# Performance work log

Hardware: AMD Instinct MI355X
Metric: run time of the kernel (lower is better)

## Reference

```python
import jax, jax.numpy as jnp
import numpy as np

B, S, HID = 1, 2048, 3584
NH, NKV, HD = 16, 8, 256
WIN = 1024                      # sliding_window_size
SOFTCAP = 50.0                  # attn_logit_softcapping
SCALING = 256 ** -0.5           # query_pre_attn_scalar ** -0.5
NEG = -2.3819763e38


def setup_inputs() -> dict:
    key = jax.random.key(0)
    k1, k2, k3 = jax.random.split(key, 3)
    hidden_states = jax.random.normal(k1, (B, S, HID), dtype=jnp.float32)
    Wqkv = jax.random.normal(k2, (HID, (NH + 2 * NKV) * HD), dtype=jnp.float32) * 0.02
    Wo = jax.random.normal(k3, (NH * HD, HID), dtype=jnp.float32) * 0.02
    # RoPE angles: freqs_cis = exp(i * pos * inv_freq), passed as cos/sin [S, HD/2]
    inv_freq = 1.0 / (10000.0 ** (jnp.arange(0, HD, 2, dtype=jnp.float32) / HD))
    ang = jnp.arange(S, dtype=jnp.float32)[:, None] * inv_freq[None, :]
    freqs_cos, freqs_sin = jnp.cos(ang), jnp.sin(ang)
    # causal additive mask [1,1,S,S]
    i = jnp.arange(S)
    mask = jnp.where(i[None, :] <= i[:, None], 0.0, NEG)[None, None, :, :].astype(jnp.float32)
    return {"hidden_states": hidden_states, "Wqkv": Wqkv, "Wo": Wo,
            "freqs_cos": freqs_cos, "freqs_sin": freqs_sin, "mask": mask}


def _rope(x, cos, sin):
    # x: [B,S,H,D]; complex mult on (first_half + i*second_half), real->first half, imag->second
    x1, x2 = jnp.split(x, 2, axis=-1)
    c = cos[None, :, None, :]
    s = sin[None, :, None, :]
    return jnp.concatenate([x1 * c - x2 * s, x1 * s + x2 * c], axis=-1)


def reference(hidden_states, Wqkv, Wo, freqs_cos, freqs_sin, mask):
    qkv = hidden_states @ Wqkv                                   # [B,S,(NH+2*NKV)*HD]
    xq, xk, xv = jnp.split(qkv, [NH * HD, (NH + NKV) * HD], axis=-1)
    xq = xq.reshape(B, S, NH, HD)
    xk = xk.reshape(B, S, NKV, HD)
    xv = xv.reshape(B, S, NKV, HD)
    xq = _rope(xq, freqs_cos, freqs_sin)
    xk = _rope(xk, freqs_cos, freqs_sin)
    g = NH // NKV                                                # GQA repeat_interleave
    k = jnp.repeat(xk, g, axis=2)                                # [B,S,NH,HD]
    v = jnp.repeat(xv, g, axis=2)
    scores = jnp.einsum('bqhd,bkhd->bhqk', xq * SCALING, k)      # [B,NH,S,S]
    # sliding-window band: triu(-W+1) * tril(W-1)  <=>  |i-j| < W
    i = jnp.arange(S)
    band = jnp.abs(i[:, None] - i[None, :]) < WIN
    m = jnp.where(band[None, None, :, :], mask, NEG)
    scores = jnp.tanh(scores / SOFTCAP) * SOFTCAP + m            # logit softcapping
    probs = jax.nn.softmax(scores.astype(jnp.float32), axis=-1).astype(xq.dtype)
    out = jnp.einsum('bhqk,bkhd->bqhd', probs, v).reshape(B, S, NH * HD)
    return out @ Wo
```

## Files before the change

kernel.cpp:

```cpp
#include <hip/hip_runtime.h>
#include <hip/hip_bf16.h>
#include <stdint.h>

#define S_LEN 2048
#define HIDDEN 3584
#define NHEAD 16
#define NKVH 8
#define HDIM 256
#define QKV_N 8192
#define AO_N 4096
#define WINLEN 1024

typedef __attribute__((ext_vector_type(8))) short bf16x8;
typedef __attribute__((ext_vector_type(4))) float f32x4;

__device__ __forceinline__ void async_cp16(const void* g, void* l) {
  __builtin_amdgcn_global_load_lds(
      (const __attribute__((address_space(1))) void*)g,
      (__attribute__((address_space(3))) void*)l, 16, 0, 0);
}

__device__ __forceinline__ float fast_exp2(float x) {
#if __has_builtin(__builtin_amdgcn_exp2f)
  return __builtin_amdgcn_exp2f(x);
#else
  return __exp2f(x);
#endif
}
__device__ __forceinline__ float fast_rcp(float x) {
#if __has_builtin(__builtin_amdgcn_rcpf)
  return __builtin_amdgcn_rcpf(x);
#else
  return 1.0f / x;
#endif
}

__device__ __forceinline__ unsigned short f2bf(float f) {
  unsigned u = __float_as_uint(f);
  u += 0x7FFF + ((u >> 16) & 1);
  return (unsigned short)(u >> 16);
}
__device__ __forceinline__ float bf2f(unsigned short h) {
  return __uint_as_float(((unsigned)h) << 16);
}

__global__ void k_cast_bf16(const float* __restrict__ in,
                            unsigned short* __restrict__ out, int n4) {
  int i = blockIdx.x * blockDim.x + threadIdx.x;
  int stride = gridDim.x * blockDim.x;
  for (; i < n4; i += stride) {
    float4 v = ((const float4*)in)[i];
    uint2 o;
    o.x = (unsigned)f2bf(v.x) | ((unsigned)f2bf(v.y) << 16);
    o.y = (unsigned)f2bf(v.z) | ((unsigned)f2bf(v.w) << 16);
    ((uint2*)out)[i] = o;
  }
}

__global__ void k_transpose_bf16(const float* __restrict__ in,
                                 unsigned short* __restrict__ out,
                                 int R, int C) {
  __shared__ float tile[64][65];
  int c0 = blockIdx.x * 64, r0 = blockIdx.y * 64;
  int t = threadIdx.x;
#pragma unroll
  for (int j = 0; j < 16; ++j) {
    int idx = t + j * 256;
    int rl = idx >> 6, cl = idx & 63;
    tile[rl][cl] = in[(size_t)(r0 + rl) * C + c0 + cl];
  }
  __syncthreads();
#pragma unroll
  for (int j = 0; j < 16; ++j) {
    int idx = t + j * 256;
    int cl = idx >> 6, rl = idx & 63;
    out[(size_t)(c0 + cl) * R + r0 + rl] = f2bf(tile[rl][cl]);
  }
}

template <bool OUT_BF16>
__global__ __launch_bounds__(256, 2) void k_gemm(
    const unsigned short* __restrict__ A, const unsigned short* __restrict__ B,
    void* __restrict__ Cout, int M, int N, int K) {
  __shared__ unsigned short sA[2][128 * 64];
  __shared__ unsigned short sB[2][128 * 64];
  const int t = threadIdx.x;
  const int lane = t & 63;
  const int wid = t >> 6;
  const int m0 = blockIdx.y * 128;
  const int n0 = blockIdx.x * 128;
  const int wr = wid >> 1, wc = wid & 1;
  const int lrow = lane & 15, lgrp = lane >> 4;

  f32x4 acc[4][4] = {};

  const int lr = lane >> 3;
  const int sw = (lane & 7) ^ (lr & 7);

  const int NT = K >> 6;

  auto stage = [&](int buf, int kt) {
    const int klo = kt * 64;
#pragma unroll
    for (int i = 0; i < 4; ++i) {
      int r = wid * 32 + i * 8 + lr;
      async_cp16(A + (size_t)(m0 + r) * K + klo + sw * 8,
                 &sA[buf][(wid * 32 + i * 8) * 64]);
    }
#pragma unroll
    for (int i = 0; i < 4; ++i) {
      int r = wid * 32 + i * 8 + lr;
      async_cp16(B + (size_t)(n0 + r) * K + klo + sw * 8,
                 &sB[buf][(wid * 32 + i * 8) * 64]);
    }
  };

  stage(0, 0);
  for (int kt = 0; kt < NT; ++kt) {
    int cur = kt & 1;
    __syncthreads();
    if (kt + 1 < NT) stage(cur ^ 1, kt + 1);
#pragma unroll
    for (int kk = 0; kk < 2; ++kk) {
      bf16x8 af[4], bfr[4];
#pragma unroll
      for (int m = 0; m < 4; ++m) {
        int r = wr * 64 + m * 16 + lrow;
        int c = (kk * 4 + lgrp) ^ (r & 7);
        af[m] = *(const bf16x8*)&sA[cur][r * 64 + c * 8];
      }
#pragma unroll
      for (int n = 0; n < 4; ++n) {
        int r = wc * 64 + n * 16 + lrow;
        int c = (kk * 4 + lgrp) ^ (r & 7);
        bfr[n] = *(const bf16x8*)&sB[cur][r * 64 + c * 8];
      }
#pragma unroll
      for (int m = 0; m < 4; ++m)
#pragma unroll
        for (int n = 0; n < 4; ++n)
          acc[m][n] = __builtin_amdgcn_mfma_f32_16x16x32_bf16(
              af[m], bfr[n], acc[m][n], 0, 0, 0);
    }
  }
#pragma unroll
  for (int m = 0; m < 4; ++m) {
    int row_b = m0 + wr * 64 + m * 16 + lgrp * 4;
#pragma unroll
    for (int n = 0; n < 4; ++n) {
      int col = n0 + wc * 64 + n * 16 + lrow;
#pragma unroll
      for (int r = 0; r < 4; ++r) {
        int row = row_b + r;
        if constexpr (OUT_BF16)
          ((unsigned short*)Cout)[(size_t)row * N + col] = f2bf(acc[m][n][r]);
        else
          ((float*)Cout)[(size_t)row * N + col] = acc[m][n][r];
      }
    }
  }
}

__global__ void k_rope_layout(const unsigned short* __restrict__ qkv,
                              const float* __restrict__ fcos,
                              const float* __restrict__ fsin,
                              unsigned short* __restrict__ Q,
                              unsigned short* __restrict__ K,
                              unsigned short* __restrict__ VT) {
  int s0 = blockIdx.x * 64;
  int y = blockIdx.y;
  int t = threadIdx.x;
  if (y < 24) {
    int colb = (y < 16) ? y * 256 : 4096 + (y - 16) * 256;
    unsigned short* out =
        (y < 16) ? (Q + (size_t)y * S_LEN * HDIM)
                 : (K + (size_t)(y - 16) * S_LEN * HDIM);
#pragma unroll 4
    for (int j = 0; j < 32; ++j) {
      int idx = t + j * 256;
      int sl = idx >> 7;
      int d = idx & 127;
      int s = s0 + sl;
      float x1 = bf2f(qkv[(size_t)s * QKV_N + colb + d]);
      float x2 = bf2f(qkv[(size_t)s * QKV_N + colb + d + 128]);
      float c = fcos[s * 128 + d], sn = fsin[s * 128 + d];
      out[(size_t)s * HDIM + d] = f2bf(x1 * c - x2 * sn);
      out[(size_t)s * HDIM + d + 128] = f2bf(x1 * sn + x2 * c);
    }
  } else {
    int kh = y - 24;
    __shared__ unsigned short tile[64][258];
#pragma unroll 4
    for (int j = 0; j < 64; ++j) {
      int idx = t + j * 256;
      int sl = idx >> 8;
      int d = idx & 255;
      tile[sl][d] = qkv[(size_t)(s0 + sl) * QKV_N + 6144 + kh * 256 + d];
    }
    __syncthreads();
    size_t base = (size_t)kh * HDIM * S_LEN + (size_t)(s0 >> 6) * (HDIM * 64);
#pragma unroll 4
    for (int j = 0; j < 64; ++j) {
      int idx = t + j * 256;
      int d = idx >> 6;
      int sl = idx & 63;
      VT[base + idx] = tile[sl][d];
    }
  }
}

__global__ __launch_bounds__(256, 2) void k_attn(
    const unsigned short* __restrict__ Q,
    const unsigned short* __restrict__ K,
    const unsigned short* __restrict__ VTB,
    unsigned short* __restrict__ O) {
  __shared__ unsigned short sK[64 * 256];
  __shared__ unsigned short sV[256 * 64];
  __shared__ unsigned short sP[4][16 * 64];
  const int t = threadIdx.x, lane = t & 63, w = t >> 6;
  const int h = blockIdx.y;
  const int r0b = blockIdx.x * 64;
  const int r0w = r0b + w * 16;
  const int lrow = lane & 15, lgrp = lane >> 4;
  const unsigned short* Qh = Q + (size_t)h * S_LEN * HDIM;
  const char* KhB = (const char*)(K + (size_t)(h >> 1) * S_LEN * HDIM);
  const char* VbB = (const char*)(VTB + (size_t)(h >> 1) * S_LEN * HDIM);

  const int cK = t & 31;
  const int rK = t >> 5;
  const int csK = (cK & 24) | ((cK ^ rK) & 7);
  const int ksrcoff = rK * 512 + csK * 16;
  const int csV = (t & 7) ^ ((t >> 3) & 7);
  const int vsrcoff = (t >> 3) * 128 + csV * 16;

  bf16x8 qf[8];
#pragma unroll
  for (int dc = 0; dc < 8; ++dc)
    qf[dc] =
        *(const bf16x8*)&Qh[(size_t)(r0w + lrow) * HDIM + dc * 32 + lgrp * 8];

  f32x4 zero4 = {0.f, 0.f, 0.f, 0.f};
  f32x4 o[16];
#pragma unroll
  for (int i = 0; i < 16; ++i) o[i] = zero4;
  float psum[4] = {0.f, 0.f, 0.f, 0.f};

  const int klo = (r0b >= 1024) ? (r0b - 1024) : 0;
  const int nsteps = ((r0b - klo) >> 6) + 1;

  const float c_pre = 0.0625f / 50.0f;
  const float c_2l2e = 2.8853900817779268f;
  const float c_l2e = 1.4426950408889634f;
  unsigned short* myP = sP[w];

  for (int step = 0; step < nsteps; ++step) {
    const int k0 = klo + step * 64;
    __syncthreads();
    {
      const char* ks = KhB + (size_t)k0 * 512;
      const char* vs = VbB + (size_t)(k0 >> 6) * 32768;
      char* dK = (char*)sK + t * 16;
      char* dV = (char*)sV + t * 16;
#pragma unroll
      for (int rr = 0; rr < 8; ++rr)
        async_cp16(ks + ksrcoff + rr * 4096, dK + rr * 4096);
#pragma unroll
      for (int rr = 0; rr < 8; ++rr)
        async_cp16(vs + vsrcoff + rr * 4096, dV + rr * 4096);
    }
    __syncthreads();

#pragma unroll
    for (int st = 0; st < 4; ++st) {
      const int row = st * 16 + lrow;
      const int rs7 = lrow & 7;
      f32x4 sa = zero4, sb = zero4;
#pragma unroll
      for (int dc = 0; dc < 4; ++dc) {
        const int La = dc * 4 + lgrp;
        const int Lb = (dc + 4) * 4 + lgrp;
        bf16x8 kfa = *(const bf16x8*)&sK[row * 256 +
                                         ((La & 24) | ((La ^ rs7) & 7)) * 8];
        bf16x8 kfb = *(const bf16x8*)&sK[row * 256 +
                                         ((Lb & 24) | ((Lb ^ rs7) & 7)) * 8];
        sa = __builtin_amdgcn_mfma_f32_16x16x32_bf16(qf[dc], kfa, sa, 0, 0, 0);
        sb = __builtin_amdgcn_mfma_f32_16x16x32_bf16(qf[dc + 4], kfb, sb, 0, 0,
                                                     0);
      }
      f32x4 s = sa + sb;
#pragma unroll
      for (int r = 0; r < 4; ++r) {
        const int q = r0w + lgrp * 4 + r;
        const int k = k0 + st * 16 + lrow;
        float tt = s[r] * c_pre;
        tt = fminf(fmaxf(tt, -10.f), 10.f);
        float z = fast_exp2(tt * c_2l2e);
        float sc = (z - 1.f) * fast_rcp(z + 1.f) * 50.f;
        float p = 0.f;
        if (k <= q && (q - k) < WINLEN)
          p = fast_exp2((sc - 50.f) * c_l2e);
        unsigned short pb = f2bf(p);
        psum[r] += bf2f(pb);
        const int qrow = lgrp * 4 + r;
        const int cc = st * 2 + (lrow >> 3);
        myP[qrow * 64 + (cc ^ (qrow & 7)) * 8 + (lrow & 7)] = pb;
      }
    }

#pragma unroll
    for (int ks2 = 0; ks2 < 2; ++ks2) {
      const int cc = ks2 * 4 + lgrp;
      bf16x8 pf = *(const bf16x8*)&myP[lrow * 64 + (cc ^ (lrow & 7)) * 8];
#pragma unroll
      for (int dt = 0; dt < 16; ++dt) {
        const int d = dt * 16 + lrow;
        bf16x8 vf = *(const bf16x8*)&sV[d * 64 + (cc ^ (lrow & 7)) * 8];
        o[dt] = __builtin_amdgcn_mfma_f32_16x16x32_bf16(pf, vf, o[dt], 0, 0, 0);
      }
    }
  }

#pragma unroll
  for (int r = 0; r < 4; ++r) {
    float v = psum[r];
    v += __shfl_xor(v, 1);
    v += __shfl_xor(v, 2);
    v += __shfl_xor(v, 4);
    v += __shfl_xor(v, 8);
    psum[r] = 1.0f / v;
  }
#pragma unroll
  for (int dt = 0; dt < 16; ++dt)
#pragma unroll
    for (int r = 0; r < 4; ++r) {
      int row = r0w + lgrp * 4 + r;
      O[(size_t)row * AO_N + h * HDIM + dt * 16 + lrow] =
          f2bf(o[dt][r] * psum[r]);
    }
}

extern "C" void kernel_launch(void* const* d_in, const int* in_sizes, int n_in,
                              void* d_out, int out_size, void* d_ws,
                              size_t ws_size, hipStream_t stream) {
  const float* hidden = (const float*)d_in[0];
  const float* Wqkv = (const float*)d_in[1];
  const float* Wo = (const float*)d_in[2];
  const float* fcos = (const float*)d_in[3];
  const float* fsin = (const float*)d_in[4];
  float* out = (float*)d_out;
  char* ws = (char*)d_ws;

  unsigned short* WqkvT = (unsigned short*)(ws + 0);
  unsigned short* hb = (unsigned short*)(ws + 58720256);
  unsigned short* qkv = (unsigned short*)(ws + 73400320);
  unsigned short* WoT = (unsigned short*)(ws + 106954752);
  unsigned short* Qb = WqkvT;
  unsigned short* Kb = WqkvT + (size_t)16 * 2048 * 256;
  unsigned short* VTb = WqkvT + (size_t)24 * 2048 * 256;
  unsigned short* AO = qkv;

  k_cast_bf16<<<1024, 256, 0, stream>>>(hidden, hb, (2048 * 3584) / 4);
  k_transpose_bf16<<<dim3(8192 / 64, 3584 / 64), 256, 0, stream>>>(
      Wqkv, WqkvT, 3584, 8192);
  k_transpose_bf16<<<dim3(3584 / 64, 4096 / 64), 256, 0, stream>>>(
      Wo, WoT, 4096, 3584);
  k_gemm<true><<<dim3(64, 16), 256, 0, stream>>>(hb, WqkvT, qkv, 2048, 8192,
                                                 3584);
  k_rope_layout<<<dim3(32, 32), 256, 0, stream>>>(qkv, fcos, fsin, Qb, Kb, VTb);
  k_attn<<<dim3(32, 16), 256, 0, stream>>>(Qb, Kb, VTb, AO);
  k_gemm<false><<<dim3(28, 16), 256, 0, stream>>>(AO, WoT, out, 2048, 3584,
                                                  4096);
}
```

Before: 564.6 us.

## Replace GEMM with larger-tile 512-thread kernel with grid swizzle and MFMA priority

Both projection GEMMs move to a new kernel with 256-wide N tiles (BM 256 for QKV, 128 for output), 8 waves per block, and a swizzled block ordering meant to improve L2 reuse. The inner loop splits fragment loads into quadrants with explicit vmcnt waits, raw barriers, and s_setprio around MFMA bursts to overlap LDS reads with matrix math. Occupancy drops to one 512-thread block per CU, and the hand-written waitcnt and barrier sequence is fragile.

```diff
diff --git a/kernel.cpp b/kernel.cpp
--- a/kernel.cpp
+++ b/kernel.cpp
@@ -42,6 +42,12 @@
 }
 __device__ __forceinline__ float bf2f(unsigned short h) {
   return __uint_as_float(((unsigned)h) << 16);
+}
+
+__device__ __forceinline__ void bar() {
+  asm volatile("" ::: "memory");
+  __builtin_amdgcn_s_barrier();
+  asm volatile("" ::: "memory");
 }
 
 __global__ void k_cast_bf16(const float* __restrict__ in,
@@ -78,84 +84,153 @@
   }
 }
 
-template <bool OUT_BF16>
-__global__ __launch_bounds__(256, 2) void k_gemm(
+template <int BM, bool OUT_BF16>
+__global__ __launch_bounds__(512, 1) void k_gemm2(
     const unsigned short* __restrict__ A, const unsigned short* __restrict__ B,
     void* __restrict__ Cout, int M, int N, int K) {
-  __shared__ unsigned short sA[2][128 * 64];
-  __shared__ unsigned short sB[2][128 * 64];
+  constexpr int M_REP = BM / 32;
+  constexpr int HM = M_REP / 2;
+  constexpr int LPK = BM / 64 + 4;
+  __shared__ unsigned short sA[2][BM * 64];
+  __shared__ unsigned short sB[2][256 * 64];
   const int t = threadIdx.x;
   const int lane = t & 63;
   const int wid = t >> 6;
-  const int m0 = blockIdx.y * 128;
-  const int n0 = blockIdx.x * 128;
-  const int wr = wid >> 1, wc = wid & 1;
+  const int wr = wid >> 2, wc = wid & 3;
   const int lrow = lane & 15, lgrp = lane >> 4;
 
-  f32x4 acc[4][4] = {};
-
-  const int lr = lane >> 3;
-  const int sw = (lane & 7) ^ (lr & 7);
+  const int gx = gridDim.x;
+  const int nwg = gx * gridDim.y;
+  const int bid = blockIdx.y * gx + blockIdx.x;
+  const int swz = (bid & 7) * (nwg >> 3) + (bid >> 3);
+  const int m0 = (swz / gx) * BM;
+  const int n0 = (swz % gx) * 256;
 
   const int NT = K >> 6;
 
-  auto stage = [&](int buf, int kt) {
-    const int klo = kt * 64;
-#pragma unroll
-    for (int i = 0; i < 4; ++i) {
-      int r = wid * 32 + i * 8 + lr;
-      async_cp16(A + (size_t)(m0 + r) * K + klo + sw * 8,
-                 &sA[buf][(wid * 32 + i * 8) * 64]);
-    }
-#pragma unroll
-    for (int i = 0; i < 4; ++i) {
-      int r = wid * 32 + i * 8 + lr;
-      async_cp16(B + (size_t)(n0 + r) * K + klo + sw * 8,
-                 &sB[buf][(wid * 32 + i * 8) * 64]);
-    }
+  const int sr = t >> 3;
+  const int scs = ((t & 7) ^ (sr & 7)) * 8;
+  auto stage = [&](int kt, int buf) {
+    const size_t kb = (size_t)kt * 64;
+    unsigned short* dA = &sA[buf][sr * 64 + (t & 7) * 8];
+    unsigned short* dB = &sB[buf][sr * 64 + (t & 7) * 8];
+#pragma unroll
+    for (int l = 0; l < BM / 64; ++l)
+      async_cp16(A + (size_t)(m0 + l * 64 + sr) * K + kb + scs,
+                 dA + l * 64 * 64);
+#pragma unroll
+    for (int l = 0; l < 4; ++l)
+      async_cp16(B + (size_t)(n0 + l * 64 + sr) * K + kb + scs,
+                 dB + l * 64 * 64);
   };
+
+  f32x4 acc[M_REP][4] = {};
 
   stage(0, 0);
   for (int kt = 0; kt < NT; ++kt) {
-    int cur = kt & 1;
-    __syncthreads();
-    if (kt + 1 < NT) stage(cur ^ 1, kt + 1);
-#pragma unroll
-    for (int kk = 0; kk < 2; ++kk) {
-      bf16x8 af[4], bfr[4];
-#pragma unroll
-      for (int m = 0; m < 4; ++m) {
-        int r = wr * 64 + m * 16 + lrow;
-        int c = (kk * 4 + lgrp) ^ (r & 7);
-        af[m] = *(const bf16x8*)&sA[cur][r * 64 + c * 8];
-      }
-#pragma unroll
-      for (int n = 0; n < 4; ++n) {
-        int r = wc * 64 + n * 16 + lrow;
-        int c = (kk * 4 + lgrp) ^ (r & 7);
-        bfr[n] = *(const bf16x8*)&sB[cur][r * 64 + c * 8];
-      }
-#pragma unroll
-      for (int m = 0; m < 4; ++m)
-#pragma unroll
-        for (int n = 0; n < 4; ++n)
-          acc[m][n] = __builtin_amdgcn_mfma_f32_16x16x32_bf16(
-              af[m], bfr[n], acc[m][n], 0, 0, 0);
-    }
-  }
-#pragma unroll
-  for (int m = 0; m < 4; ++m) {
-    int row_b = m0 + wr * 64 + m * 16 + lgrp * 4;
-#pragma unroll
-    for (int n = 0; n < 4; ++n) {
-      int col = n0 + wc * 64 + n * 16 + lrow;
+    const int buf = kt & 1;
+    if (kt + 1 < NT) {
+      stage(kt + 1, buf ^ 1);
+      if constexpr (LPK == 8)
+        asm volatile("s_waitcnt vmcnt(8)" ::: "memory");
+      else
+        asm volatile("s_waitcnt vmcnt(6)" ::: "memory");
+    } else {
+      asm volatile("s_waitcnt vmcnt(0)" ::: "memory");
+    }
+    bar();
+
+    const unsigned short* a = sA[buf];
+    const unsigned short* b = sB[buf];
+    auto ldA = [&](int mf, int kk) {
+      return *(const bf16x8*)&a[(wr * (BM / 2) + mf * 16 + lrow) * 64 +
+                                (((kk * 4 + lgrp)) ^ (lrow & 7)) * 8];
+    };
+    auto ldB = [&](int nf, int kk) {
+      return *(const bf16x8*)&b[(wc * 64 + nf * 16 + lrow) * 64 +
+                                (((kk * 4 + lgrp)) ^ (lrow & 7)) * 8];
+    };
+
+    bf16x8 aA[HM][2], bB0[2][2], bB1[2][2];
+#pragma unroll
+    for (int i = 0; i < HM; ++i) {
+      aA[i][0] = ldA(i, 0);
+      aA[i][1] = ldA(i, 1);
+    }
+#pragma unroll
+    for (int j = 0; j < 2; ++j) {
+      bB0[j][0] = ldB(j, 0);
+      bB0[j][1] = ldB(j, 1);
+    }
+    __builtin_amdgcn_s_setprio(1);
+#pragma unroll
+    for (int i = 0; i < HM; ++i)
+#pragma unroll
+      for (int j = 0; j < 2; ++j)
+#pragma unroll
+        for (int kk = 0; kk < 2; ++kk)
+          acc[i][j] = __builtin_amdgcn_mfma_f32_16x16x32_bf16(
+              aA[i][kk], bB0[j][kk], acc[i][j], 0, 0, 0);
+    __builtin_amdgcn_s_setprio(0);
+    bar();
+#pragma unroll
+    for (int j = 0; j < 2; ++j) {
+      bB1[j][0] = ldB(2 + j, 0);
+      bB1[j][1] = ldB(2 + j, 1);
+    }
+    __builtin_amdgcn_s_setprio(1);
+#pragma unroll
+    for (int i = 0; i < HM; ++i)
+#pragma unroll
+      for (int j = 0; j < 2; ++j)
+#pragma unroll
+        for (int kk = 0; kk < 2; ++kk)
+          acc[i][2 + j] = __builtin_amdgcn_mfma_f32_16x16x32_bf16(
+              aA[i][kk], bB1[j][kk], acc[i][2 + j], 0, 0, 0);
+    __builtin_amdgcn_s_setprio(0);
+    bar();
+#pragma unroll
+    for (int i = 0; i < HM; ++i) {
+      aA[i][0] = ldA(HM + i, 0);
+      aA[i][1] = ldA(HM + i, 1);
+    }
+    __builtin_amdgcn_s_setprio(1);
+#pragma unroll
+    for (int i = 0; i < HM; ++i)
+#pragma unroll
+      for (int j = 0; j < 2; ++j)
+#pragma unroll
+        for (int kk = 0; kk < 2; ++kk)
+          acc[HM + i][2 + j] = __builtin_amdgcn_mfma_f32_16x16x32_bf16(
+              aA[i][kk], bB1[j][kk], acc[HM + i][2 + j], 0, 0, 0);
+    __builtin_amdgcn_s_setprio(0);
+    bar();
+    __builtin_amdgcn_s_setprio(1);
+#pragma unroll
+    for (int i = 0; i < HM; ++i)
+#pragma unroll
+      for (int j = 0; j < 2; ++j)
+#pragma unroll
+        for (int kk = 0; kk < 2; ++kk)
+          acc[HM + i][j] = __builtin_amdgcn_mfma_f32_16x16x32_bf16(
+              aA[i][kk], bB0[j][kk], acc[HM + i][j], 0, 0, 0);
+    __builtin_amdgcn_s_setprio(0);
+    bar();
+  }
+
+#pragma unroll
+  for (int mf = 0; mf < M_REP; ++mf) {
+    int row_b = m0 + wr * (BM / 2) + mf * 16 + lgrp * 4;
+#pragma unroll
+    for (int nf = 0; nf < 4; ++nf) {
+      int col = n0 + wc * 64 + nf * 16 + lrow;
 #pragma unroll
       for (int r = 0; r < 4; ++r) {
         int row = row_b + r;
         if constexpr (OUT_BF16)
-          ((unsigned short*)Cout)[(size_t)row * N + col] = f2bf(acc[m][n][r]);
+          ((unsigned short*)Cout)[(size_t)row * N + col] = f2bf(acc[mf][nf][r]);
         else
-          ((float*)Cout)[(size_t)row * N + col] = acc[m][n][r];
+          ((float*)Cout)[(size_t)row * N + col] = acc[mf][nf][r];
       }
     }
   }
@@ -364,10 +439,10 @@
       Wqkv, WqkvT, 3584, 8192);
   k_transpose_bf16<<<dim3(3584 / 64, 4096 / 64), 256, 0, stream>>>(
       Wo, WoT, 4096, 3584);
-  k_gemm<true><<<dim3(64, 16), 256, 0, stream>>>(hb, WqkvT, qkv, 2048, 8192,
-                                                 3584);
+  k_gemm2<256, true><<<dim3(8192 / 256, 2048 / 256), 512, 0, stream>>>(
+      hb, WqkvT, qkv, 2048, 8192, 3584);
   k_rope_layout<<<dim3(32, 32), 256, 0, stream>>>(qkv, fcos, fsin, Qb, Kb, VTb);
   k_attn<<<dim3(32, 16), 256, 0, stream>>>(Qb, Kb, VTb, AO);
-  k_gemm<false><<<dim3(28, 16), 256, 0, stream>>>(AO, WoT, out, 2048, 3584,
-                                                  4096);
-}
+  k_gemm2<128, false><<<dim3(3584 / 256, 2048 / 128), 512, 0, stream>>>(
+      AO, WoT, out, 2048, 3584, 4096);
+}
```

Result: slower. 589.3 us (+4.4%).
